# Performance work log

Measured on AMD Instinct MI355X. Metric: run time of the kernel, lower is better.

The kernel has to match this reference:

```python
import jax, jax.numpy as jnp
import numpy as np

D = 64
NEG = 0.01            # leakyrelu_neg_slope
X_CONN = 0.25         # x_connection_init
SKIP_H = 0.5          # skip_weight_h
SIGMAS = np.asarray(1.5 ** np.arange(15), np.float32)  # all_sigmas_dist

N_LIG, N_REC = 4096, 8192
E_LIG, E_REC = 65536, 262144
F_LIG, F_REC, NRBF = 15, 27, 15


def _lrelu(x):
    return jax.nn.leaky_relu(x, NEG)


def _ln(x, g, b, eps=1e-5):
    m = x.mean(-1, keepdims=True)
    v = ((x - m) ** 2).mean(-1, keepdims=True)
    return (x - m) * jax.lax.rsqrt(v + eps) * g + b


def _mlp2(x, w1, b1, g, bt, w2, b2):
    # nn.Sequential(Linear, Dropout(0), LeakyReLU, LayerNorm, Linear) in eval mode
    return _ln(_lrelu(x @ w1 + b1), g, bt) @ w2 + b2


def _coords_mlp(m, w1, b1, w2, b2):
    # nn.Sequential(Linear, Dropout(0), LeakyReLU, Linear(out,1))
    return _lrelu(m @ w1 + b1) @ w2 + b2  # [E, 1]


def _seg_mean(v, idx, n):
    # DGL fn.mean over incoming edges at destination nodes (0 for isolated nodes)
    s = jax.ops.segment_sum(v, idx, num_segments=n)
    c = jax.ops.segment_sum(jnp.ones(idx.shape, v.dtype), idx, num_segments=n)
    return s / jnp.maximum(c, 1.0)[:, None]


def setup_inputs() -> dict:
    key = jax.random.key(0)
    ks = iter(jax.random.split(key, 64))

    def n(shape, s=1.0):
        return jax.random.normal(next(ks), shape, jnp.float32) * s

    def lin(i, o):
        return n((i, o), 1.0 / float(np.sqrt(i)))

    zeros = lambda *s: jnp.zeros(s, jnp.float32)
    ones = lambda *s: jnp.ones(s, jnp.float32)

    d = {}
    d['coords_lig'] = n((N_LIG, 3))
    d['h_lig'] = n((N_LIG, D))
    d['orig_h_lig'] = n((N_LIG, D))
    d['orig_coords_lig'] = n((N_LIG, 3))
    d['coords_rec'] = n((N_REC, 3))
    d['h_rec'] = n((N_REC, D))
    d['orig_h_rec'] = n((N_REC, D))
    d['orig_coords_rec'] = n((N_REC, 3))
    d['lig_src'] = jax.random.randint(next(ks), (E_LIG,), 0, N_LIG)
    d['lig_dst'] = jax.random.randint(next(ks), (E_LIG,), 0, N_LIG)
    d['lig_efeat'] = n((E_LIG, F_LIG))
    d['rec_src'] = jax.random.randint(next(ks), (E_REC,), 0, N_REC)
    d['rec_dst'] = jax.random.randint(next(ks), (E_REC,), 0, N_REC)
    d['rec_efeat'] = n((E_REC, F_REC))
    d['mask'] = (jax.random.uniform(next(ks), (N_LIG, N_REC)) < 0.5).astype(jnp.float32)
    # ---- parameters ----
    d['lig_em_w1'], d['lig_em_b1'] = lin(2 * D + F_LIG + NRBF, D), zeros(D)
    d['lig_em_g'], d['lig_em_bt'] = ones(D), zeros(D)
    d['lig_em_w2'], d['lig_em_b2'] = lin(D, D), zeros(D)
    d['rec_em_w1'], d['rec_em_b1'] = lin(2 * D + F_REC + NRBF, D), zeros(D)
    d['rec_em_g'], d['rec_em_bt'] = ones(D), zeros(D)
    d['rec_em_w2'], d['rec_em_b2'] = lin(D, D), zeros(D)
    d['lig_cm_w1'], d['lig_cm_b1'] = lin(D, D), zeros(D)
    d['lig_cm_w2'], d['lig_cm_b2'] = lin(D, 1), zeros(1)
    d['rec_cm_w1'], d['rec_cm_b1'] = lin(D, D), zeros(D)
    d['rec_cm_w2'], d['rec_cm_b2'] = lin(D, 1), zeros(1)
    for nm in ['q_lig_w', 'k_lig_w', 'v_lig_w', 'q_rec_w', 'k_rec_w', 'v_rec_w']:
        d[nm] = lin(D, D)
    d['lig_nm_w1'], d['lig_nm_b1'] = lin(4 * D, D), zeros(D)
    d['lig_nm_g'], d['lig_nm_bt'] = ones(D), zeros(D)
    d['lig_nm_w2'], d['lig_nm_b2'] = lin(D, D), zeros(D)
    d['rec_nm_w1'], d['rec_nm_b1'] = lin(4 * D, D), zeros(D)
    d['rec_nm_g'], d['rec_nm_bt'] = ones(D), zeros(D)
    d['rec_nm_w2'], d['rec_nm_b2'] = lin(D, D), zeros(D)
    return d


def reference(coords_lig, h_lig, orig_h_lig, orig_coords_lig,
              coords_rec, h_rec, orig_h_rec, orig_coords_rec,
              lig_src, lig_dst, lig_efeat, rec_src, rec_dst, rec_efeat, mask,
              lig_em_w1, lig_em_b1, lig_em_g, lig_em_bt, lig_em_w2, lig_em_b2,
              rec_em_w1, rec_em_b1, rec_em_g, rec_em_bt, rec_em_w2, rec_em_b2,
              lig_cm_w1, lig_cm_b1, lig_cm_w2, lig_cm_b2,
              rec_cm_w1, rec_cm_b1, rec_cm_w2, rec_cm_b2,
              q_lig_w, k_lig_w, v_lig_w, q_rec_w, k_rec_w, v_rec_w,
              lig_nm_w1, lig_nm_b1, lig_nm_g, lig_nm_bt, lig_nm_w2, lig_nm_b2,
              rec_nm_w1, rec_nm_b1, rec_nm_g, rec_nm_bt, rec_nm_w2, rec_nm_b2):
    n_lig, n_rec = coords_lig.shape[0], coords_rec.shape[0]
    sig = jnp.asarray(SIGMAS, coords_lig.dtype)

    # --- ligand edge messages: x_rel = x_src - x_dst, multi-scale RBF of |x_rel|^2 ---
    xr_l = coords_lig[lig_src] - coords_lig[lig_dst]                       # [E_l, 3]
    rbf_l = jnp.exp(-jnp.sum(xr_l * xr_l, -1, keepdims=True) / sig)        # [E_l, 15]
    msg_l = _mlp2(jnp.concatenate([h_lig[lig_src], h_lig[lig_dst], lig_efeat, rbf_l], -1),
                  lig_em_w1, lig_em_b1, lig_em_g, lig_em_bt, lig_em_w2, lig_em_b2)

    # --- receptor edge messages (rec_square_distance_scale = 1) ---
    xr_r = coords_rec[rec_src] - coords_rec[rec_dst]
    rbf_r = jnp.exp(-jnp.sum(xr_r * xr_r, -1, keepdims=True) / sig)
    msg_r = _mlp2(jnp.concatenate([h_rec[rec_src], h_rec[rec_dst], rec_efeat, rbf_r], -1),
                  rec_em_w1, rec_em_b1, rec_em_g, rec_em_bt, rec_em_w2, rec_em_b2)

    # --- masked cross-graph attention (pre/post cross-msg norms are identity) ---
    q_l, k_l, v_l = _lrelu(h_lig @ q_lig_w), _lrelu(h_lig @ k_lig_w), h_lig @ v_lig_w
    q_r, k_r, v_r = _lrelu(h_rec @ q_rec_w), _lrelu(h_rec @ k_rec_w), h_rec @ v_rec_w
    s_lr = mask * (q_l @ k_r.T) - 1000.0 * (1.0 - mask)
    att_l = jax.nn.softmax(s_lr, axis=1) @ v_r                             # [N_l, D]
    mt = mask.T
    s_rl = mt * (q_r @ k_l.T) - 1000.0 * (1.0 - mt)
    att_r = jax.nn.softmax(s_rl, axis=1) @ v_l                             # [N_r, D]

    # --- equivariant coordinate update: mean_j phi_x(m_ij) * x_rel, + skip to orig ---
    coef_l = _coords_mlp(msg_l, lig_cm_w1, lig_cm_b1, lig_cm_w2, lig_cm_b2)
    x_lig = X_CONN * orig_coords_lig + (1.0 - X_CONN) * coords_lig + _seg_mean(xr_l * coef_l, lig_dst, n_lig)
    coef_r = _coords_mlp(msg_r, rec_cm_w1, rec_cm_b1, rec_cm_w2, rec_cm_b2)
    x_rec = X_CONN * orig_coords_rec + (1.0 - X_CONN) * coords_rec + _seg_mean(xr_r * coef_r, rec_dst, n_rec)

    # --- node feature update with skip (h_feats_dim == out_feats_dim) ---
    aggr_l = _seg_mean(msg_l, lig_dst, n_lig)
    h_lig_out = SKIP_H * _mlp2(jnp.concatenate([h_lig, aggr_l, att_l, orig_h_lig], -1),
                               lig_nm_w1, lig_nm_b1, lig_nm_g, lig_nm_bt, lig_nm_w2, lig_nm_b2) \
        + (1.0 - SKIP_H) * h_lig
    aggr_r = _seg_mean(msg_r, rec_dst, n_rec)
    h_rec_out = SKIP_H * _mlp2(jnp.concatenate([h_rec, aggr_r, att_r, orig_h_rec], -1),
                               rec_nm_w1, rec_nm_b1, rec_nm_g, rec_nm_bt, rec_nm_w2, rec_nm_b2) \
        + (1.0 - SKIP_H) * h_rec
    return x_lig, h_lig_out, x_rec, h_rec_out
```

## Files before the change

kernel.cpp:

```cpp
#include <hip/hip_runtime.h>
#include <hip/hip_bf16.h>

typedef __hip_bfloat16 bf16;
typedef __attribute__((ext_vector_type(8))) short bfrag8;
typedef __attribute__((ext_vector_type(4))) float f32x4;

#define N_LIG 4096
#define N_REC 8192
#define E_LIG 65536
#define E_REC 262144
#define F_LIGc 15
#define F_RECc 27

__device__ __forceinline__ float ldkv(const float* p, size_t i) { return p[i]; }
__device__ __forceinline__ float ldkv(const bf16* p, size_t i) { return __bfloat162float(p[i]); }
__device__ __forceinline__ short bfbits(float x) {
    bf16 b = __float2bfloat16(x);
    return *(short*)&b;
}
__device__ __forceinline__ unsigned short stg(const float* p, size_t i) {
    return (unsigned short)bfbits(p[i]);
}
__device__ __forceinline__ unsigned short stg(const bf16* p, size_t i) {
    return *(const unsigned short*)(p + i);
// ... 21 lines not shown
    0.1316872428f, 0.08779149520f, 0.05852766346f, 0.03901844231f,
    0.02601229487f, 0.01734152992f, 0.01156101994f, 0.007707346628f,
    0.005138231085f, 0.003425487390f};

__device__ __forceinline__ float wave_sum(float v) {
    #pragma unroll
    for (int o = 32; o > 0; o >>= 1) v += __shfl_xor(v, o, 64);
    return v;
}
__device__ __forceinline__ float quad_max(float v) {
    v = fmaxf(v, __shfl_xor(v, 1)); v = fmaxf(v, __shfl_xor(v, 2));
    v = fmaxf(v, __shfl_xor(v, 4)); v = fmaxf(v, __shfl_xor(v, 8));
    return v;
}

__global__ void zero_kernel(float* __restrict__ p, int n) {
    int i = blockIdx.x * blockDim.x + threadIdx.x;
    if (i < n) p[i] = 0.f;
}

__global__ void cvt4_kernel(
    const float* __restrict__ a, bf16* __restrict__ oa, int na,
    const float* __restrict__ b, bf16* __restrict__ ob, int nb,
    const float* __restrict__ c, bf16* __restrict__ oc, int nc,
    const float* __restrict__ d, bf16* __restrict__ od, int nd)
{
    int i = blockIdx.x * 256 + threadIdx.x;
    if (i < na) { oa[i] = __float2bfloat16(a[i]); return; }
    i -= na;
    if (i < nb) { ob[i] = __float2bfloat16(b[i]); return; }
    i -= nb;
    if (i < nc) { oc[i] = __float2bfloat16(c[i]); return; }
    i -= nc;
    if (i < nd) od[i] = __float2bfloat16(d[i]);
}

__global__ void hist2_kernel(const int* __restrict__ dl, const int* __restrict__ dr,
                             int* __restrict__ cl, int* __restrict__ cr) {
    int i = blockIdx.x * 256 + threadIdx.x;
    if (i < E_LIG) { atomicAdd(&cl[dl[i]], 1); return; }
    i -= E_LIG;
    if (i < E_REC) atomicAdd(&cr[dr[i]], 1);
}

__global__ __launch_bounds__(256) void scan2_kernel(
    const int* __restrict__ cl, int* __restrict__ curl,
    const int* __restrict__ cr, int* __restrict__ curr)
{
    const int* counts = blockIdx.x ? cr : cl;
    int* cursor = blockIdx.x ? curr : curl;
    int n = blockIdx.x ? N_REC : N_LIG;
    __shared__ int part[256];
    int t = threadIdx.x;
    int c = n / 256;
    int base = t * c;
    int s = 0;
    for (int i = 0; i < c; ++i) s += counts[base + i];
// ... 7 lines not shown
    }
    int run = part[t] - s;
    for (int i = 0; i < c; ++i) {
        cursor[base + i] = run;
        run += counts[base + i];
    }
}

__global__ void scatter2_kernel(const int* __restrict__ dl, const int* __restrict__ dr,
                                int* __restrict__ curl, int* __restrict__ curr,
                                int* __restrict__ ordl, int* __restrict__ ordr) {
    int i = blockIdx.x * 256 + threadIdx.x;
    if (i < E_LIG) { ordl[atomicAdd(&curl[dl[i]], 1)] = i; return; }
    i -= E_LIG;
    if (i < E_REC) ordr[atomicAdd(&curr[dr[i]], 1)] = i;
}

__global__ __launch_bounds__(256) void pack_frags(
    const float* __restrict__ w_rec1, const float* __restrict__ w_lig1,
    const float* __restrict__ w_rec2, const float* __restrict__ w_lig2,
    const float* __restrict__ c_rec1, const float* __restrict__ c_lig1,
    unsigned short* __restrict__ p_rec1, unsigned short* __restrict__ p_lig1,
    unsigned short* __restrict__ p_rec2, unsigned short* __restrict__ p_lig2,
    unsigned short* __restrict__ pc_rec1, unsigned short* __restrict__ pc_lig1)
{
    int b = blockIdx.x;
    const float* src; unsigned short* dst; int kk, IN;
    if (b < 6)       { src = w_rec1; dst = p_rec1;  kk = b;      IN = 170; }
    else if (b < 11) { src = w_lig1; dst = p_lig1;  kk = b - 6;  IN = 158; }
    else if (b < 13) { src = w_rec2; dst = p_rec2;  kk = b - 11; IN = 64; }
    else if (b < 15) { src = w_lig2; dst = p_lig2;  kk = b - 13; IN = 64; }
    else if (b < 17) { src = c_rec1; dst = pc_rec1; kk = b - 15; IN = 64; }
    else             { src = c_lig1; dst = pc_lig1; kk = b - 17; IN = 64; }
    int t = threadIdx.x, wv = t >> 6, L = t & 63, lm = L & 15, qd = L >> 4;
    int n = wv * 16 + lm;
    unsigned short tmp[8];
    #pragma unroll
    for (int j = 0; j < 8; ++j) {
        int k = kk * 32 + qd * 8 + j;
        tmp[j] = (k < IN) ? (unsigned short)bfbits(src[k * 64 + n]) : (unsigned short)0;
    }
    *(uint4*)&dst[((size_t)(kk * 4 + wv) * 64 + L) * 8] = *(uint4*)tmp;
}

template <int F, int K1S, typename HT>
__device__ __forceinline__ void edge_body(
    char* sbuf, int ebid,
    const int* __restrict__ order,
    const float* __restrict__ coords, const HT* __restrict__ h,
    const int* __restrict__ src, const int* __restrict__ dst,
    const HT* __restrict__ efeat,
    const unsigned short* __restrict__ w1p, const float* __restrict__ b1,
    const float* __restrict__ g, const float* __restrict__ bt,
    const unsigned short* __restrict__ w2p, const float* __restrict__ b2,
    const unsigned short* __restrict__ c1p, const float* __restrict__ cb1,
    const float* __restrict__ cw2, const float* __restrict__ cb2,
    float* __restrict__ aggr, float* __restrict__ xacc)
// ... 220 lines not shown
    const float *h, *qw, *mf;
    const bf16 *kkp, *vvp;
    const unsigned long long* mq;
    long mrs, mcs;
    float *pO, *pM, *pL;
    int n_rows, n_cols, nsplit;
    if (bid < nb1) {
        h = h1; qw = qw1; kkp = k1; vvp = v1; mq = mq1; mf = mf1; mrs = mrs1; mcs = mcs1;
        pO = pO1; pM = pM1; pL = pL1; n_rows = nrows1; n_cols = ncols1; nsplit = nsplit1;
    } else {
        h = h2; qw = qw2; kkp = k2; vvp = v2; mq = mq2; mf = mf2; mrs = mrs2; mcs = mcs2;
        pO = pO2; pM = pM2; pL = pL2; n_rows = nrows2; n_cols = ncols2; nsplit = nsplit2;
        bid -= nb1;
    }

    unsigned short* sQ = (unsigned short*)sbuf;
    unsigned short* sP = (unsigned short*)(sbuf + 8192);
    unsigned short* sK = (unsigned short*)(sbuf + 16384);
    unsigned short* sV = (unsigned short*)(sbuf + 24576);
    uint2* mtq = (uint2*)(sbuf + 32768);
    unsigned char* mt = (unsigned char*)(sbuf + 32768);

    const int t  = threadIdx.x;
    const int wv = t >> 6;
    const int lm = t & 15;
    const int qd = (t & 63) >> 4;
    const int rb = bid / nsplit;
    const int sp = bid - rb * nsplit;
    const int r0 = rb * 64;
    const int cols_per = n_cols / nsplit;
    const int c_begin = sp * cols_per;

    const int cP = t >> 3, segP = (t & 7) * 8;

    #pragma unroll
    for (int u = 0; u < 2; ++u) {
// ... 6 lines not shown
        const float* qp = qw + (size_t)rr * 64 + segP;
        #pragma unroll
        for (int j = 0; j < 8; ++j) sK[swz(segP + j, rr)] = bfbits(qp[j]);
    }

    uint4 kreg[2], vreg[2];
    unsigned long long mregq = 0;
    kreg[0] = *(const uint4*)(kkp + (size_t)(c_begin + cP) * 64 + segP);
    kreg[1] = *(const uint4*)(kkp + (size_t)(c_begin + cP + 32) * 64 + segP);
    vreg[0] = *(const uint4*)(vvp + (size_t)(c_begin + cP) * 64 + segP);
    vreg[1] = *(const uint4*)(vvp + (size_t)(c_begin + cP + 32) * 64 + segP);
    if (MMODE == 0 && t < 64)
        mregq = mq[(size_t)(c_begin >> 6) * n_rows + r0 + t];
    __syncthreads();

    {
        bfrag8 a0 = *(const bfrag8*)&sP[swz(wv * 16 + lm, qd * 8)];
        bfrag8 a1 = *(const bfrag8*)&sP[swz(wv * 16 + lm, 32 + qd * 8)];
        #pragma unroll
        for (int ns = 0; ns < 4; ++ns) {
            f32x4 acc = {0.f, 0.f, 0.f, 0.f};
            bfrag8 b0 = *(const bfrag8*)&sK[swz(ns * 16 + lm, qd * 8)];
            bfrag8 b1 = *(const bfrag8*)&sK[swz(ns * 16 + lm, 32 + qd * 8)];
            acc = __builtin_amdgcn_mfma_f32_16x16x32_bf16(a0, b0, acc, 0, 0, 0);
            acc = __builtin_amdgcn_mfma_f32_16x16x32_bf16(a1, b1, acc, 0, 0, 0);
            #pragma unroll
            for (int r = 0; r < 4; ++r) {
                float v = acc[r];
                v = v > 0.f ? v : 0.01f * v;
                sQ[swz(wv * 16 + qd * 4 + r, ns * 16 + lm)] = bfbits(v);
            }
        }
    }
    __syncthreads();

    float rm[4];
    #pragma unroll
    for (int r = 0; r < 4; ++r) rm[r] = -1e30f;
    f32x4 o[4];
    #pragma unroll
    for (int ds = 0; ds < 4; ++ds) o[ds] = (f32x4){0.f, 0.f, 0.f, 0.f};
    f32x4 osum = {0.f, 0.f, 0.f, 0.f};
    const short ONE = (short)0x3F80;
    const bfrag8 bones = {ONE, ONE, ONE, ONE, ONE, ONE, ONE, ONE};

    const int nt = cols_per / 64;
    for (int tile = 0; tile < nt; ++tile) {
        #pragma unroll
        for (int u = 0; u < 2; ++u) {
// ... 22 lines not shown
            }
        }
        __syncthreads();

        if (tile + 1 < nt) {
            int c0n = c_begin + (tile + 1) * 64;
            kreg[0] = *(const uint4*)(kkp + (size_t)(c0n + cP) * 64 + segP);
            kreg[1] = *(const uint4*)(kkp + (size_t)(c0n + cP + 32) * 64 + segP);
            vreg[0] = *(const uint4*)(vvp + (size_t)(c0n + cP) * 64 + segP);
            vreg[1] = *(const uint4*)(vvp + (size_t)(c0n + cP + 32) * 64 + segP);
            if (MMODE == 0 && t < 64)
                mregq = mq[(size_t)(c0n >> 6) * n_rows + r0 + t];
        }

        f32x4 s[4];
        {
            bfrag8 a0 = *(const bfrag8*)&sQ[swz(wv * 16 + lm, qd * 8)];
            bfrag8 a1 = *(const bfrag8*)&sQ[swz(wv * 16 + lm, 32 + qd * 8)];
            #pragma unroll
            for (int ns = 0; ns < 4; ++ns) {
                f32x4 acc = {0.f, 0.f, 0.f, 0.f};
                bfrag8 b0 = *(const bfrag8*)&sK[swz(ns * 16 + lm, qd * 8)];
                bfrag8 b1 = *(const bfrag8*)&sK[swz(ns * 16 + lm, 32 + qd * 8)];
                acc = __builtin_amdgcn_mfma_f32_16x16x32_bf16(a0, b0, acc, 0, 0, 0);
                acc = __builtin_amdgcn_mfma_f32_16x16x32_bf16(a1, b1, acc, 0, 0, 0);
                s[ns] = acc;
            }
        }

        float alpha[4];
        #pragma unroll
        for (int r = 0; r < 4; ++r) {
            int rloc = wv * 16 + qd * 4 + r;
            float v0, v1, v2, v3;
            if (MMODE == 0) {
                uint2 w = mtq[rloc];
                v0 = (w.x >> lm) & 1        ? s[0][r] : -1000.f;
                v1 = (w.x >> (16 + lm)) & 1 ? s[1][r] : -1000.f;
                v2 = (w.y >> lm) & 1        ? s[2][r] : -1000.f;
                v3 = (w.y >> (16 + lm)) & 1 ? s[3][r] : -1000.f;
            } else {
                v0 = mt[rloc * 80 +  0 + lm] ? s[0][r] : -1000.f;
// ... 42 lines not shown
        #pragma unroll
        for (int r = 0; r < 4; ++r) {
            int row = r0 + wv * 16 + qd * 4 + r;
            pO[((size_t)sp * n_rows + row) * 64 + ds * 16 + lm] = o[ds][r];
        }
    if (lm == 0) {
        #pragma unroll
        for (int r = 0; r < 4; ++r) {
            int row = r0 + wv * 16 + qd * 4 + r;
            pM[(size_t)sp * n_rows + row] = rm[r];
            pL[(size_t)sp * n_rows + row] = osum[r];
        }
    }
}

__global__ __launch_bounds__(256, 4) void mega_kernel(
    int nb1,
    const float* h1, const float* qw1, const bf16* k1, const bf16* v1,
    const unsigned long long* mq1, float* pO1, float* pM1, float* pL1,
    int nrows1, int ncols1, int ns1,
    const float* h2, const float* qw2, const bf16* k2, const bf16* v2,
    const unsigned long long* mq2, float* pO2, float* pM2, float* pL2,
    int nrows2, int ncols2, int ns2,
    const int* ordR, const float* coordsR, const bf16* hR,
    const int* srcR, const int* dstR, const bf16* efR,
    const unsigned short* w1pR, const float* b1R, const float* gR, const float* btR,
    const unsigned short* w2pR, const float* b2R,
    const unsigned short* c1pR, const float* cb1R, const float* cw2R, const float* cb2R,
    float* aggrR, float* xaccR,
    const int* ordL, const float* coordsL, const bf16* hL,
    const int* srcL, const int* dstL, const bf16* efL,
    const unsigned short* w1pL, const float* b1L, const float* gL, const float* btL,
    const unsigned short* w2pL, const float* b2L,
    const unsigned short* c1pL, const float* cb1L, const float* cw2L, const float* cb2L,
    float* aggrL, float* xaccL)
{
    __shared__ __align__(16) char sbuf[33280];
    int bid = blockIdx.x;
    int g7 = bid / 7, r7 = bid - g7 * 7;
    if (r7 < 2) {
        attn_body<0>(sbuf, g7 * 2 + r7, nb1,
            h1, qw1, k1, v1, mq1, (const float*)0, 0L, 0L, pO1, pM1, pL1, nrows1, ncols1, ns1,
            h2, qw2, k2, v2, mq2, (const float*)0, 0L, 0L, pO2, pM2, pL2, nrows2, ncols2, ns2);
    } else {
        int eid = g7 * 5 + (r7 - 2);
        if (eid < E_REC / 64)
            edge_body<F_RECc, 6, bf16>(sbuf, eid, ordR, coordsR, hR, srcR, dstR, efR,
                w1pR, b1R, gR, btR, w2pR, b2R, c1pR, cb1R, cw2R, cb2R, aggrR, xaccR);
        else
            edge_body<F_LIGc, 5, bf16>(sbuf, eid - E_REC / 64, ordL, coordsL, hL, srcL, dstL, efL,
                w1pL, b1L, gL, btL, w2pL, b2L, c1pL, cb1L, cw2L, cb2L, aggrL, xaccL);
    }
// ... 10 lines not shown
{
    __shared__ __align__(16) char sbuf[64 * (K1S * 32 + 8) * 2 + 5632];
    edge_body<F, K1S, float>(sbuf, blockIdx.x, order, coords, h, src, dst, efeat,
        w1p, b1, g, bt, w2p, b2, c1p, cb1, cw2, cb2, aggr, xacc);
}

__global__ __launch_bounds__(256, 4) void attn_f32mask(
    int nb1,
    const float* h1, const float* qw1, const bf16* k1, const bf16* v1,
    const float* mf1, long mrs1, long mcs1,
    float* pO1, float* pM1, float* pL1, int nrows1, int ncols1, int ns1,
    const float* h2, const float* qw2, const bf16* k2, const bf16* v2,
    const float* mf2, long mrs2, long mcs2,
    float* pO2, float* pM2, float* pL2, int nrows2, int ncols2, int ns2)
{
    __shared__ __align__(16) char sbuf[37888];
    attn_body<1>(sbuf, blockIdx.x, nb1,
        h1, qw1, k1, v1, (const unsigned long long*)0, mf1, mrs1, mcs1,
        pO1, pM1, pL1, nrows1, ncols1, ns1,
        h2, qw2, k2, v2, (const unsigned long long*)0, mf2, mrs2, mcs2,
        pO2, pM2, pL2, nrows2, ncols2, ns2);
}

__global__ __launch_bounds__(256, 3) void node_mfma(
    int nbl, int nbn,
    const float* h1, const float* __restrict__ aggr1, const int* __restrict__ cnt1,
    const float* att1, const float* __restrict__ origh1,
    const float* __restrict__ w1a, const float* __restrict__ b1a,
    const float* __restrict__ ga, const float* __restrict__ bta,
    const float* __restrict__ w2a, const float* __restrict__ b2a, float* out1,
    const float* h2, const float* __restrict__ aggr2, const int* __restrict__ cnt2,
// ... 132 lines not shown
    #pragma unroll
    for (int m = 0; m < 4; ++m) {
        f32x4 acc = {0.f, 0.f, 0.f, 0.f};
        #pragma unroll
        for (int kk = 0; kk < 2; ++kk) {
            bfrag8 a = *(const bfrag8*)&h1b[(m * 16 + lm) * 72 + kk * 32 + qd * 8];
            acc = __builtin_amdgcn_mfma_f32_16x16x32_bf16(a, w2f[kk], acc, 0, 0, 0);
        }
        #pragma unroll
        for (int r = 0; r < 4; ++r) {
            int row = n0 + m * 16 + qd * 4 + r;
            float o = acc[r] + b2n;
            float hv = h[(size_t)row * 64 + n];
            h_out[(size_t)row * 64 + n] = 0.5f * o + 0.5f * hv;
        }
    }
}

__global__ __launch_bounds__(256) void kv_proj_kernel(
    const float* __restrict__ h_lig, const float* __restrict__ h_rec,
    const float* __restrict__ kwl, const float* __restrict__ vwl,
    const float* __restrict__ kwr, const float* __restrict__ vwr,
    bf16* __restrict__ kbl, bf16* __restrict__ vbl,
    bf16* __restrict__ kbr, bf16* __restrict__ vbr)
{
    int job = blockIdx.x * 4 + (threadIdx.x >> 6);
    int j = threadIdx.x & 63;
    const float *h, *w; bf16* out; int node, do_l;
    if (job < N_LIG)                { h = h_lig; w = kwl; out = kbl; node = job;                   do_l = 1; }
    else if (job < 2 * N_LIG)       { h = h_lig; w = vwl; out = vbl; node = job - N_LIG;           do_l = 0; }
    else if (job < 2 * N_LIG + N_REC) { h = h_rec; w = kwr; out = kbr; node = job - 2 * N_LIG;     do_l = 1; }
    else                            { h = h_rec; w = vwr; out = vbr; node = job - 2 * N_LIG - N_REC; do_l = 0; }
    float xv = h[(size_t)node * 64 + j];
    float acc = 0.f;
    #pragma unroll
    for (int i = 0; i < 64; ++i) acc += __shfl(xv, i, 64) * w[i * 64 + j];
    if (do_l) acc = acc > 0.f ? acc : 0.01f * acc;
    out[(size_t)node * 64 + j] = __float2bfloat16(acc);
}

__global__ __launch_bounds__(256) void build_masks(
    const float* __restrict__ mask, unsigned long long* __restrict__ mq,
    unsigned long long* __restrict__ mqT, int R, int C)
{
    __shared__ __align__(4) unsigned char tr[64 * 68];
    __shared__ __align__(4) unsigned char tc[64 * 68];
    int r0 = blockIdx.y * 64, c0 = blockIdx.x * 64;
    int t = threadIdx.x;
    int cs = (t & 15) * 4;
    #pragma unroll
    for (int rr = 0; rr < 4; ++rr) {
        int r = (t >> 4) + rr * 16;
        const float* mp = &mask[(size_t)(r0 + r) * C + c0 + cs];
        unsigned char b0 = mp[0] != 0.f, b1 = mp[1] != 0.f;
        unsigned char b2 = mp[2] != 0.f, b3 = mp[3] != 0.f;
        tr[r * 68 + cs + 0] = b0; tr[r * 68 + cs + 1] = b1;
        tr[r * 68 + cs + 2] = b2; tr[r * 68 + cs + 3] = b3;
        tc[(cs + 0) * 68 + r] = b0; tc[(cs + 1) * 68 + r] = b1;
        tc[(cs + 2) * 68 + r] = b2; tc[(cs + 3) * 68 + r] = b3;
    }
    __syncthreads();
    if (t < 128) {
        const unsigned* p = (t < 64) ? (const unsigned*)&tr[t * 68]
                                     : (const unsigned*)&tc[(t - 64) * 68];
        unsigned lo = 0, hi = 0;
        #pragma unroll
        for (int i = 0; i < 8; ++i)
            lo |= (((p[i] & 0x01010101u) * 0x01020408u) >> 24 & 0xFu) << (4 * i);
        #pragma unroll
        for (int i = 8; i < 16; ++i)
            hi |= (((p[i] & 0x01010101u) * 0x01020408u) >> 24 & 0xFu) << (4 * (i - 8));
        unsigned long long w = (unsigned long long)lo | ((unsigned long long)hi << 32);
        if (t < 64) mq[(size_t)(c0 >> 6) * R + r0 + t] = w;
        else        mqT[(size_t)(r0 >> 6) * C + c0 + (t - 64)] = w;
    }
}

__global__ __launch_bounds__(64) void attn_merge2(
    const float* __restrict__ pO1, const float* __restrict__ pM1, const float* __restrict__ pL1,
    float* __restrict__ out1, int ns1,
    const float* __restrict__ pO2, const float* __restrict__ pM2, const float* __restrict__ pL2,
    float* __restrict__ out2, int ns2)
{
    int r = blockIdx.x;
    const float *pO, *pM, *pL; float* out; int n_rows, nsplit;
    if (r < N_LIG) { pO = pO1; pM = pM1; pL = pL1; out = out1; n_rows = N_LIG; nsplit = ns1; }
    else { r -= N_LIG; pO = pO2; pM = pM2; pL = pL2; out = out2; n_rows = N_REC; nsplit = ns2; }
    int d = threadIdx.x;
    float mstar = -1e30f;
// ... 105 lines not shown
    const float *k_rec_w = (const float*)d_in[39], *v_rec_w = (const float*)d_in[40];
    const float *lig_nm_w1 = (const float*)d_in[41], *lig_nm_b1 = (const float*)d_in[42];
    const float *lig_nm_g  = (const float*)d_in[43], *lig_nm_bt = (const float*)d_in[44];
    const float *lig_nm_w2 = (const float*)d_in[45], *lig_nm_b2 = (const float*)d_in[46];
    const float *rec_nm_w1 = (const float*)d_in[47], *rec_nm_b1 = (const float*)d_in[48];
    const float *rec_nm_g  = (const float*)d_in[49], *rec_nm_bt = (const float*)d_in[50];
    const float *rec_nm_w2 = (const float*)d_in[51], *rec_nm_b2 = (const float*)d_in[52];

    char* wsb = (char*)d_ws;
    float* aggr_l = (float*)(wsb + 16);
    float* aggr_r = aggr_l + (size_t)N_LIG * 64;
    float* xacc_l = aggr_r + (size_t)N_REC * 64;
    float* xacc_r = xacc_l + (size_t)N_LIG * 3;
    int* counts_l = (int*)(xacc_r + (size_t)N_REC * 3);
    int* counts_r = counts_l + N_LIG;
    const size_t zero_floats =
        (size_t)N_LIG * 64 + (size_t)N_REC * 64 + N_LIG * 3 + N_REC * 3 + N_LIG + N_REC;
    int* cursor_l = counts_r + N_REC;
    int* cursor_r = cursor_l + N_LIG;
    int* order_l  = cursor_r + N_REC;
    int* order_r  = order_l + E_LIG;
    unsigned short* p_rec1  = (unsigned short*)(order_r + E_REC);
    unsigned short* p_lig1  = p_rec1 + 6 * 2048;
    unsigned short* p_rec2  = p_lig1 + 5 * 2048;
    unsigned short* p_lig2  = p_rec2 + 2 * 2048;
    unsigned short* pc_rec1 = p_lig2 + 2 * 2048;
    unsigned short* pc_lig1 = pc_rec1 + 2 * 2048;
    char* kv_base = (char*)(pc_lig1 + 2 * 2048);
    const size_t core_b = (size_t)(kv_base - wsb);
    const size_t kv_b = (size_t)(N_LIG + N_REC) * 64 * 2 * 2;

    const size_t mq1_n = (size_t)(N_REC / 64) * N_LIG;
// ... 28 lines not shown
    float* pM2 = pL1 + (size_t)ns1 * N_LIG;
    float* pL2 = pM2 + (size_t)ns2 * N_REC;
    unsigned long long* mqb  = (unsigned long long*)(kv_base + kv_b + part_b);
    unsigned long long* mqbT = mqb + mq1_n;
    bf16* hb_l  = (bf16*)(mqbT + mq2_n);
    bf16* hb_r  = hb_l + (size_t)N_LIG * 64;
    bf16* efb_l = hb_r + (size_t)N_REC * 64;
    bf16* efb_r = efb_l + (size_t)E_LIG * F_LIGc;

    float* out = (float*)d_out;
    float* x_lig_o = out;
    float* h_lig_o = out + 12288;
    float* x_rec_o = out + 274432;
    float* h_rec_o = out + 299008;

    zero_kernel<<<((int)zero_floats + 255) / 256, 256, 0, stream>>>(aggr_l, (int)zero_floats);

    if (tier == 0) {
        dim3 bg(N_REC / 64, N_LIG / 64);
        build_masks<<<bg, 256, 0, stream>>>(mask, mqb, mqbT, N_LIG, N_REC);
    }

    pack_frags<<<19, 256, 0, stream>>>(
        rec_em_w1, lig_em_w1, rec_em_w2, lig_em_w2, rec_cm_w1, lig_cm_w1,
        p_rec1, p_lig1, p_rec2, p_lig2, pc_rec1, pc_lig1);

    hist2_kernel<<<(E_LIG + E_REC) / 256, 256, 0, stream>>>(lig_dst, rec_dst, counts_l, counts_r);
    scan2_kernel<<<2, 256, 0, stream>>>(counts_l, cursor_l, counts_r, cursor_r);
    scatter2_kernel<<<(E_LIG + E_REC) / 256, 256, 0, stream>>>(
        lig_dst, rec_dst, cursor_l, cursor_r, order_l, order_r);

    kv_proj_kernel<<<(2 * (N_LIG + N_REC)) / 4, 256, 0, stream>>>(
        h_lig, h_rec, k_lig_w, v_lig_w, k_rec_w, v_rec_w,
        kb_l, vb_l, kb_r, vb_r);

    const int nb1 = (N_LIG / 64) * ns1;
    const int nb2 = (N_REC / 64) * ns2;

    if (tier == 0) {
        cvt4_kernel<<<(N_LIG * 64 + N_REC * 64 + E_LIG * F_LIGc + E_REC * F_RECc + 255) / 256,
                      256, 0, stream>>>(
            h_lig, hb_l, N_LIG * 64, h_rec, hb_r, N_REC * 64,
            lig_efeat, efb_l, E_LIG * F_LIGc, rec_efeat, efb_r, E_REC * F_RECc);

        mega_kernel<<<7 * 1024, 256, 0, stream>>>(
            nb1,
            h_lig, q_lig_w, kb_r, vb_r, mqb, pO1, pM1, pL1, N_LIG, N_REC, ns1,
            h_rec, q_rec_w, kb_l, vb_l, mqbT, pO2, pM2, pL2, N_REC, N_LIG, ns2,
            order_r, coords_rec, hb_r, rec_src, rec_dst, efb_r,
            p_rec1, rec_em_b1, rec_em_g, rec_em_bt, p_rec2, rec_em_b2,
            pc_rec1, rec_cm_b1, rec_cm_w2, rec_cm_b2, aggr_r, xacc_r,
            order_l, coords_lig, hb_l, lig_src, lig_dst, efb_l,
            p_lig1, lig_em_b1, lig_em_g, lig_em_bt, p_lig2, lig_em_b2,
            pc_lig1, lig_cm_b1, lig_cm_w2, lig_cm_b2, aggr_l, xacc_l);

        attn_merge2<<<N_LIG + N_REC, 64, 0, stream>>>(
            pO1, pM1, pL1, h_lig_o, ns1, pO2, pM2, pL2, h_rec_o, ns2);
    } else {
        edge_mfma_f<F_LIGc, 5><<<E_LIG / 64, 256, 0, stream>>>(
            order_l, coords_lig, h_lig, lig_src, lig_dst, lig_efeat,
            p_lig1, lig_em_b1, lig_em_g, lig_em_bt, p_lig2, lig_em_b2,
            pc_lig1, lig_cm_b1, lig_cm_w2, lig_cm_b2, aggr_l, xacc_l);
        edge_mfma_f<F_RECc, 6><<<E_REC / 64, 256, 0, stream>>>(
            order_r, coords_rec, h_rec, rec_src, rec_dst, rec_efeat,
            p_rec1, rec_em_b1, rec_em_g, rec_em_bt, p_rec2, rec_em_b2,
            pc_rec1, rec_cm_b1, rec_cm_w2, rec_cm_b2, aggr_r, xacc_r);
        if (tier == 1) {
            attn_f32mask<<<nb1 + nb2, 256, 0, stream>>>(
                nb1,
                h_lig, q_lig_w, kb_r, vb_r, mask, (long)N_REC, 1L,
                pO1, pM1, pL1, N_LIG, N_REC, ns1,
                h_rec, q_rec_w, kb_l, vb_l, mask, 1L, (long)N_REC,
                pO2, pM2, pL2, N_REC, N_LIG, ns2);
// ... 22 lines not shown
```

Baseline: 605.7 us.

## Fuse preprocessing kernels into one launch and shrink attention shared memory

Merges mask bit-packing, bf16 conversion, K/V projection, destination histogram and weight fragment packing into a single prep_kernel on the default tier, cutting several launches and their serialization gaps. The attention body now keeps the Q tile as register fragments loaded once, reusing the sP buffer instead of a separate sQ region. That shrinks shared memory so mega_kernel can raise launch bounds to 5 blocks per CU. The cost is higher register pressure from keeping the Q fragments resident, which may cause spills under the tighter occupancy bound.

```diff
diff --git a/kernel.cpp b/kernel.cpp
--- a/kernel.cpp
+++ b/kernel.cpp
@@ -59,33 +59,180 @@
     return v;
 }
 
+__device__ __forceinline__ void pack_body(
+    int b, int t,
+    const float* w_rec1, const float* w_lig1, const float* w_rec2, const float* w_lig2,
+    const float* c_rec1, const float* c_lig1,
+    unsigned short* p_rec1, unsigned short* p_lig1,
+    unsigned short* p_rec2, unsigned short* p_lig2,
+    unsigned short* pc_rec1, unsigned short* pc_lig1)
+{
+    const float* src; unsigned short* dst; int kk, IN;
+    if (b < 6)       { src = w_rec1; dst = p_rec1;  kk = b;      IN = 170; }
+    else if (b < 11) { src = w_lig1; dst = p_lig1;  kk = b - 6;  IN = 158; }
+    else if (b < 13) { src = w_rec2; dst = p_rec2;  kk = b - 11; IN = 64; }
+    else if (b < 15) { src = w_lig2; dst = p_lig2;  kk = b - 13; IN = 64; }
+    else if (b < 17) { src = c_rec1; dst = pc_rec1; kk = b - 15; IN = 64; }
+    else             { src = c_lig1; dst = pc_lig1; kk = b - 17; IN = 64; }
+    int wv = t >> 6, L = t & 63, lm = L & 15, qd = L >> 4;
+    int n = wv * 16 + lm;
+    unsigned short tmp[8];
+    #pragma unroll
+    for (int j = 0; j < 8; ++j) {
+        int k = kk * 32 + qd * 8 + j;
+        tmp[j] = (k < IN) ? (unsigned short)bfbits(src[k * 64 + n]) : (unsigned short)0;
+    }
+    *(uint4*)&dst[((size_t)(kk * 4 + wv) * 64 + L) * 8] = *(uint4*)tmp;
+}
+
+__device__ __forceinline__ void kv_body(
+    int job, int j,
+    const float* h_lig, const float* h_rec,
+    const float* kwl, const float* vwl, const float* kwr, const float* vwr,
+    bf16* kbl, bf16* vbl, bf16* kbr, bf16* vbr)
+{
+    const float *h, *w; bf16* out; int node, do_l;
+    if (job < N_LIG)                  { h = h_lig; w = kwl; out = kbl; node = job;                     do_l = 1; }
+    else if (job < 2 * N_LIG)         { h = h_lig; w = vwl; out = vbl; node = job - N_LIG;             do_l = 0; }
+    else if (job < 2 * N_LIG + N_REC) { h = h_rec; w = kwr; out = kbr; node = job - 2 * N_LIG;         do_l = 1; }
+    else                              { h = h_rec; w = vwr; out = vbr; node = job - 2 * N_LIG - N_REC; do_l = 0; }
+    float xv = h[(size_t)node * 64 + j];
+    float acc = 0.f;
+    #pragma unroll
+    for (int i = 0; i < 64; ++i) acc += __shfl(xv, i, 64) * w[i * 64 + j];
+    if (do_l) acc = acc > 0.f ? acc : 0.01f * acc;
+    out[(size_t)node * 64 + j] = __float2bfloat16(acc);
+}
+
+__device__ __forceinline__ void mask_body(
+    unsigned char* tr, unsigned char* tc, int bx, int by, int t,
+    const float* mask, unsigned long long* mq, unsigned long long* mqT, int R, int C)
+{
+    int r0 = by * 64, c0 = bx * 64;
+    int cs = (t & 15) * 4;
+    #pragma unroll
+    for (int rr = 0; rr < 4; ++rr) {
+        int r = (t >> 4) + rr * 16;
+        const float* mp = &mask[(size_t)(r0 + r) * C + c0 + cs];
+        unsigned char b0 = mp[0] != 0.f, b1 = mp[1] != 0.f;
+        unsigned char b2 = mp[2] != 0.f, b3 = mp[3] != 0.f;
+        tr[r * 68 + cs + 0] = b0; tr[r * 68 + cs + 1] = b1;
+        tr[r * 68 + cs + 2] = b2; tr[r * 68 + cs + 3] = b3;
+        tc[(cs + 0) * 68 + r] = b0; tc[(cs + 1) * 68 + r] = b1;
+        tc[(cs + 2) * 68 + r] = b2; tc[(cs + 3) * 68 + r] = b3;
+    }
+    __syncthreads();
+    if (t < 128) {
+        const unsigned* p = (t < 64) ? (const unsigned*)&tr[t * 68]
+                                     : (const unsigned*)&tc[(t - 64) * 68];
+        unsigned lo = 0, hi = 0;
+        #pragma unroll
+        for (int i = 0; i < 8; ++i)
+            lo |= (((p[i] & 0x01010101u) * 0x01020408u) >> 24 & 0xFu) << (4 * i);
+        #pragma unroll
+        for (int i = 8; i < 16; ++i)
+            hi |= (((p[i] & 0x01010101u) * 0x01020408u) >> 24 & 0xFu) << (4 * (i - 8));
+        unsigned long long w = (unsigned long long)lo | ((unsigned long long)hi << 32);
+        if (t < 64) mq[(size_t)(c0 >> 6) * R + r0 + t] = w;
+        else        mqT[(size_t)(r0 >> 6) * C + c0 + (t - 64)] = w;
+    }
+}
+
+#define NB_MASK  ((N_REC / 64) * (N_LIG / 64))
+#define N_CVT    (N_LIG * 64 + N_REC * 64 + E_LIG * F_LIGc + E_REC * F_RECc)
+#define NB_CVT   (N_CVT / 256)
+#define NB_KV    (2 * (N_LIG + N_REC) / 4)
+#define N_ZERO   (N_LIG * 64 + N_REC * 64 + N_LIG * 3 + N_REC * 3 + N_LIG + N_REC)
+#define NB_HIST  ((E_LIG + E_REC) / 256)
+#define NB_PACK  19
+#define NB_PREP  (NB_MASK + NB_CVT + NB_KV + NB_HIST + NB_PACK)
+
+__global__ __launch_bounds__(256) void prep_kernel(
+    const float* __restrict__ mask, unsigned long long* __restrict__ mq,
+    unsigned long long* __restrict__ mqT,
+    const float* __restrict__ h_lig, bf16* __restrict__ hb_l,
+    const float* __restrict__ h_rec, bf16* __restrict__ hb_r,
+    const float* __restrict__ ef_l, bf16* __restrict__ efb_l,
+    const float* __restrict__ ef_r, bf16* __restrict__ efb_r,
+    const float* __restrict__ kwl, const float* __restrict__ vwl,
+    const float* __restrict__ kwr, const float* __restrict__ vwr,
+    bf16* __restrict__ kbl, bf16* __restrict__ vbl,
+    bf16* __restrict__ kbr, bf16* __restrict__ vbr,
+    const int* __restrict__ dl, const int* __restrict__ dr,
+    int* __restrict__ cl, int* __restrict__ cr,
+    const float* w_rec1, const float* w_lig1, const float* w_rec2, const float* w_lig2,
+    const float* c_rec1, const float* c_lig1,
+    unsigned short* p_rec1, unsigned short* p_lig1,
+    unsigned short* p_rec2, unsigned short* p_lig2,
+    unsigned short* pc_rec1, unsigned short* pc_lig1)
+{
+    __shared__ unsigned char tr[64 * 68];
+    __shared__ unsigned char tc[64 * 68];
+    int b = blockIdx.x, t = threadIdx.x;
+    if (b < NB_MASK) {
+        mask_body(tr, tc, b & 127, b >> 7, t, mask, mq, mqT, N_LIG, N_REC);
+        return;
+    }
+    b -= NB_MASK;
+    if (b < NB_CVT) {
+        int i = b * 256 + t;
+        if (i < N_LIG * 64) { hb_l[i] = __float2bfloat16(h_lig[i]); return; }
+        i -= N_LIG * 64;
+        if (i < N_REC * 64) { hb_r[i] = __float2bfloat16(h_rec[i]); return; }
+        i -= N_REC * 64;
+        if (i < E_LIG * F_LIGc) { efb_l[i] = __float2bfloat16(ef_l[i]); return; }
+        i -= E_LIG * F_LIGc;
+        efb_r[i] = __float2bfloat16(ef_r[i]);
+        return;
+    }
+    b -= NB_CVT;
+    if (b < NB_KV) {
+        kv_body(b * 4 + (t >> 6), t & 63, h_lig, h_rec, kwl, vwl, kwr, vwr,
+                kbl, vbl, kbr, vbr);
+        return;
+    }
+    b -= NB_KV;
+    if (b < NB_HIST) {
+        int i = b * 256 + t;
+        if (i < E_LIG) atomicAdd(&cl[dl[i]], 1);
+        else atomicAdd(&cr[dr[i - E_LIG]], 1);
+        return;
+    }
+    b -= NB_HIST;
+    pack_body(b, t, w_rec1, w_lig1, w_rec2, w_lig2, c_rec1, c_lig1,
+              p_rec1, p_lig1, p_rec2, p_lig2, pc_rec1, pc_lig1);
+}
+
 __global__ void zero_kernel(float* __restrict__ p, int n) {
     int i = blockIdx.x * blockDim.x + threadIdx.x;
     if (i < n) p[i] = 0.f;
 }
-
-__global__ void cvt4_kernel(
-    const float* __restrict__ a, bf16* __restrict__ oa, int na,
-    const float* __restrict__ b, bf16* __restrict__ ob, int nb,
-    const float* __restrict__ c, bf16* __restrict__ oc, int nc,
-    const float* __restrict__ d, bf16* __restrict__ od, int nd)
-{
-    int i = blockIdx.x * 256 + threadIdx.x;
-    if (i < na) { oa[i] = __float2bfloat16(a[i]); return; }
-    i -= na;
-    if (i < nb) { ob[i] = __float2bfloat16(b[i]); return; }
-    i -= nb;
-    if (i < nc) { oc[i] = __float2bfloat16(c[i]); return; }
-    i -= nc;
-    if (i < nd) od[i] = __float2bfloat16(d[i]);
-}
-
 __global__ void hist2_kernel(const int* __restrict__ dl, const int* __restrict__ dr,
                              int* __restrict__ cl, int* __restrict__ cr) {
     int i = blockIdx.x * 256 + threadIdx.x;
     if (i < E_LIG) { atomicAdd(&cl[dl[i]], 1); return; }
     i -= E_LIG;
     if (i < E_REC) atomicAdd(&cr[dr[i]], 1);
+}
+__global__ __launch_bounds__(256) void pack_frags(
+    const float* w_rec1, const float* w_lig1, const float* w_rec2, const float* w_lig2,
+    const float* c_rec1, const float* c_lig1,
+    unsigned short* p_rec1, unsigned short* p_lig1,
+    unsigned short* p_rec2, unsigned short* p_lig2,
+    unsigned short* pc_rec1, unsigned short* pc_lig1)
+{
+    pack_body(blockIdx.x, threadIdx.x, w_rec1, w_lig1, w_rec2, w_lig2, c_rec1, c_lig1,
+              p_rec1, p_lig1, p_rec2, p_lig2, pc_rec1, pc_lig1);
+}
+__global__ __launch_bounds__(256) void kv_proj_kernel(
+    const float* __restrict__ h_lig, const float* __restrict__ h_rec,
+    const float* __restrict__ kwl, const float* __restrict__ vwl,
+    const float* __restrict__ kwr, const float* __restrict__ vwr,
+    bf16* __restrict__ kbl, bf16* __restrict__ vbl,
+    bf16* __restrict__ kbr, bf16* __restrict__ vbr)
+{
+    kv_body(blockIdx.x * 4 + (threadIdx.x >> 6), threadIdx.x & 63,
+            h_lig, h_rec, kwl, vwl, kwr, vwr, kbl, vbl, kbr, vbr);
 }
 
 __global__ __launch_bounds__(256) void scan2_kernel(
@@ -123,33 +270,6 @@
     if (i < E_LIG) { ordl[atomicAdd(&curl[dl[i]], 1)] = i; return; }
     i -= E_LIG;
     if (i < E_REC) ordr[atomicAdd(&curr[dr[i]], 1)] = i;
-}
-
-__global__ __launch_bounds__(256) void pack_frags(
-    const float* __restrict__ w_rec1, const float* __restrict__ w_lig1,
-    const float* __restrict__ w_rec2, const float* __restrict__ w_lig2,
-    const float* __restrict__ c_rec1, const float* __restrict__ c_lig1,
-    unsigned short* __restrict__ p_rec1, unsigned short* __restrict__ p_lig1,
-    unsigned short* __restrict__ p_rec2, unsigned short* __restrict__ p_lig2,
-    unsigned short* __restrict__ pc_rec1, unsigned short* __restrict__ pc_lig1)
-{
-    int b = blockIdx.x;
-    const float* src; unsigned short* dst; int kk, IN;
-    if (b < 6)       { src = w_rec1; dst = p_rec1;  kk = b;      IN = 170; }
-    else if (b < 11) { src = w_lig1; dst = p_lig1;  kk = b - 6;  IN = 158; }
-    else if (b < 13) { src = w_rec2; dst = p_rec2;  kk = b - 11; IN = 64; }
-    else if (b < 15) { src = w_lig2; dst = p_lig2;  kk = b - 13; IN = 64; }
-    else if (b < 17) { src = c_rec1; dst = pc_rec1; kk = b - 15; IN = 64; }
-    else             { src = c_lig1; dst = pc_lig1; kk = b - 17; IN = 64; }
-    int t = threadIdx.x, wv = t >> 6, L = t & 63, lm = L & 15, qd = L >> 4;
-    int n = wv * 16 + lm;
-    unsigned short tmp[8];
-    #pragma unroll
-    for (int j = 0; j < 8; ++j) {
-        int k = kk * 32 + qd * 8 + j;
-        tmp[j] = (k < IN) ? (unsigned short)bfbits(src[k * 64 + n]) : (unsigned short)0;
-    }
-    *(uint4*)&dst[((size_t)(kk * 4 + wv) * 64 + L) * 8] = *(uint4*)tmp;
 }
 
 template <int F, int K1S, typename HT>
@@ -400,12 +520,11 @@
         bid -= nb1;
     }
 
-    unsigned short* sQ = (unsigned short*)sbuf;
-    unsigned short* sP = (unsigned short*)(sbuf + 8192);
-    unsigned short* sK = (unsigned short*)(sbuf + 16384);
-    unsigned short* sV = (unsigned short*)(sbuf + 24576);
-    uint2* mtq = (uint2*)(sbuf + 32768);
-    unsigned char* mt = (unsigned char*)(sbuf + 32768);
+    unsigned short* sP = (unsigned short*)sbuf;
+    unsigned short* sK = (unsigned short*)(sbuf + 8192);
+    unsigned short* sV = (unsigned short*)(sbuf + 16384);
+    uint2* mtq = (uint2*)(sbuf + 24576);
+    unsigned char* mt = (unsigned char*)(sbuf + 24576);
 
     const int t  = threadIdx.x;
     const int wv = t >> 6;
@@ -442,6 +561,7 @@
         mregq = mq[(size_t)(c_begin >> 6) * n_rows + r0 + t];
     __syncthreads();
 
+    float qv[4][4];
     {
         bfrag8 a0 = *(const bfrag8*)&sP[swz(wv * 16 + lm, qd * 8)];
         bfrag8 a1 = *(const bfrag8*)&sP[swz(wv * 16 + lm, 32 + qd * 8)];
@@ -455,12 +575,20 @@
             #pragma unroll
             for (int r = 0; r < 4; ++r) {
                 float v = acc[r];
-                v = v > 0.f ? v : 0.01f * v;
-                sQ[swz(wv * 16 + qd * 4 + r, ns * 16 + lm)] = bfbits(v);
+                qv[ns][r] = v > 0.f ? v : 0.01f * v;
             }
         }
     }
     __syncthreads();
+
+    #pragma unroll
+    for (int ns = 0; ns < 4; ++ns)
+        #pragma unroll
+        for (int r = 0; r < 4; ++r)
+            sP[swz(wv * 16 + qd * 4 + r, ns * 16 + lm)] = bfbits(qv[ns][r]);
+    __syncthreads();
+    bfrag8 aq0 = *(const bfrag8*)&sP[swz(wv * 16 + lm, qd * 8)];
+    bfrag8 aq1 = *(const bfrag8*)&sP[swz(wv * 16 + lm, 32 + qd * 8)];
 
     float rm[4];
     #pragma unroll
@@ -513,18 +641,14 @@
         }
 
         f32x4 s[4];
-        {
-            bfrag8 a0 = *(const bfrag8*)&sQ[swz(wv * 16 + lm, qd * 8)];
-            bfrag8 a1 = *(const bfrag8*)&sQ[swz(wv * 16 + lm, 32 + qd * 8)];
-            #pragma unroll
-            for (int ns = 0; ns < 4; ++ns) {
-                f32x4 acc = {0.f, 0.f, 0.f, 0.f};
-                bfrag8 b0 = *(const bfrag8*)&sK[swz(ns * 16 + lm, qd * 8)];
-                bfrag8 b1 = *(const bfrag8*)&sK[swz(ns * 16 + lm, 32 + qd * 8)];
-                acc = __builtin_amdgcn_mfma_f32_16x16x32_bf16(a0, b0, acc, 0, 0, 0);
-                acc = __builtin_amdgcn_mfma_f32_16x16x32_bf16(a1, b1, acc, 0, 0, 0);
-                s[ns] = acc;
-            }
+        #pragma unroll
+        for (int ns = 0; ns < 4; ++ns) {
+            f32x4 acc = {0.f, 0.f, 0.f, 0.f};
+            bfrag8 b0 = *(const bfrag8*)&sK[swz(ns * 16 + lm, qd * 8)];
+            bfrag8 b1 = *(const bfrag8*)&sK[swz(ns * 16 + lm, 32 + qd * 8)];
+            acc = __builtin_amdgcn_mfma_f32_16x16x32_bf16(aq0, b0, acc, 0, 0, 0);
+            acc = __builtin_amdgcn_mfma_f32_16x16x32_bf16(aq1, b1, acc, 0, 0, 0);
+            s[ns] = acc;
         }
 
         float alpha[4];
@@ -597,7 +721,7 @@
     }
 }
 
-__global__ __launch_bounds__(256, 4) void mega_kernel(
+__global__ __launch_bounds__(256, 5) void mega_kernel(
     int nb1,
     const float* h1, const float* qw1, const bf16* k1, const bf16* v1,
     const unsigned long long* mq1, float* pO1, float* pM1, float* pL1,
@@ -618,7 +742,7 @@
     const unsigned short* c1pL, const float* cb1L, const float* cw2L, const float* cb2L,
     float* aggrL, float* xaccL)
 {
-    __shared__ __align__(16) char sbuf[33280];
+    __shared__ __align__(16) char sbuf[31232];
     int bid = blockIdx.x;
     int g7 = bid / 7, r7 = bid - g7 * 7;
     if (r7 < 2) {
@@ -659,7 +783,7 @@
     const float* mf2, long mrs2, long mcs2,
     float* pO2, float* pM2, float* pL2, int nrows2, int ncols2, int ns2)
 {
-    __shared__ __align__(16) char sbuf[37888];
+    __shared__ __align__(16) char sbuf[29696];
     attn_body<1>(sbuf, blockIdx.x, nb1,
         h1, qw1, k1, v1, (const unsigned long long*)0, mf1, mrs1, mcs1,
         pO1, pM1, pL1, nrows1, ncols1, ns1,
@@ -822,65 +946,6 @@
             float hv = h[(size_t)row * 64 + n];
             h_out[(size_t)row * 64 + n] = 0.5f * o + 0.5f * hv;
         }
-    }
-}
-
-__global__ __launch_bounds__(256) void kv_proj_kernel(
-    const float* __restrict__ h_lig, const float* __restrict__ h_rec,
-    const float* __restrict__ kwl, const float* __restrict__ vwl,
-    const float* __restrict__ kwr, const float* __restrict__ vwr,
-    bf16* __restrict__ kbl, bf16* __restrict__ vbl,
-    bf16* __restrict__ kbr, bf16* __restrict__ vbr)
-{
-    int job = blockIdx.x * 4 + (threadIdx.x >> 6);
-    int j = threadIdx.x & 63;
-    const float *h, *w; bf16* out; int node, do_l;
-    if (job < N_LIG)                { h = h_lig; w = kwl; out = kbl; node = job;                   do_l = 1; }
-    else if (job < 2 * N_LIG)       { h = h_lig; w = vwl; out = vbl; node = job - N_LIG;           do_l = 0; }
-    else if (job < 2 * N_LIG + N_REC) { h = h_rec; w = kwr; out = kbr; node = job - 2 * N_LIG;     do_l = 1; }
-    else                            { h = h_rec; w = vwr; out = vbr; node = job - 2 * N_LIG - N_REC; do_l = 0; }
-    float xv = h[(size_t)node * 64 + j];
-    float acc = 0.f;
-    #pragma unroll
-    for (int i = 0; i < 64; ++i) acc += __shfl(xv, i, 64) * w[i * 64 + j];
-    if (do_l) acc = acc > 0.f ? acc : 0.01f * acc;
-    out[(size_t)node * 64 + j] = __float2bfloat16(acc);
-}
-
-__global__ __launch_bounds__(256) void build_masks(
-    const float* __restrict__ mask, unsigned long long* __restrict__ mq,
-    unsigned long long* __restrict__ mqT, int R, int C)
-{
-    __shared__ __align__(4) unsigned char tr[64 * 68];
-    __shared__ __align__(4) unsigned char tc[64 * 68];
-    int r0 = blockIdx.y * 64, c0 = blockIdx.x * 64;
-    int t = threadIdx.x;
-    int cs = (t & 15) * 4;
-    #pragma unroll
-    for (int rr = 0; rr < 4; ++rr) {
-        int r = (t >> 4) + rr * 16;
-        const float* mp = &mask[(size_t)(r0 + r) * C + c0 + cs];
-        unsigned char b0 = mp[0] != 0.f, b1 = mp[1] != 0.f;
-        unsigned char b2 = mp[2] != 0.f, b3 = mp[3] != 0.f;
-        tr[r * 68 + cs + 0] = b0; tr[r * 68 + cs + 1] = b1;
-        tr[r * 68 + cs + 2] = b2; tr[r * 68 + cs + 3] = b3;
-        tc[(cs + 0) * 68 + r] = b0; tc[(cs + 1) * 68 + r] = b1;
-        tc[(cs + 2) * 68 + r] = b2; tc[(cs + 3) * 68 + r] = b3;
-    }
-    __syncthreads();
-    if (t < 128) {
-        const unsigned* p = (t < 64) ? (const unsigned*)&tr[t * 68]
-                                     : (const unsigned*)&tc[(t - 64) * 68];
-        unsigned lo = 0, hi = 0;
-        #pragma unroll
-        for (int i = 0; i < 8; ++i)
-            lo |= (((p[i] & 0x01010101u) * 0x01020408u) >> 24 & 0xFu) << (4 * i);
-        #pragma unroll
-        for (int i = 8; i < 16; ++i)
-            hi |= (((p[i] & 0x01010101u) * 0x01020408u) >> 24 & 0xFu) << (4 * (i - 8));
-        unsigned long long w = (unsigned long long)lo | ((unsigned long long)hi << 32);
-        if (t < 64) mq[(size_t)(c0 >> 6) * R + r0 + t] = w;
-        else        mqT[(size_t)(r0 >> 6) * C + c0 + (t - 64)] = w;
     }
 }
 
@@ -1016,8 +1081,6 @@
     float* xacc_r = xacc_l + (size_t)N_LIG * 3;
     int* counts_l = (int*)(xacc_r + (size_t)N_REC * 3);
     int* counts_r = counts_l + N_LIG;
-    const size_t zero_floats =
-        (size_t)N_LIG * 64 + (size_t)N_REC * 64 + N_LIG * 3 + N_REC * 3 + N_LIG + N_REC;
     int* cursor_l = counts_r + N_REC;
     int* cursor_r = cursor_l + N_LIG;
     int* order_l  = cursor_r + N_REC;
@@ -1076,34 +1139,21 @@
     float* x_rec_o = out + 274432;
     float* h_rec_o = out + 299008;
 
-    zero_kernel<<<((int)zero_floats + 255) / 256, 256, 0, stream>>>(aggr_l, (int)zero_floats);
-
-    if (tier == 0) {
-        dim3 bg(N_REC / 64, N_LIG / 64);
-        build_masks<<<bg, 256, 0, stream>>>(mask, mqb, mqbT, N_LIG, N_REC);
-    }
-
-    pack_frags<<<19, 256, 0, stream>>>(
-        rec_em_w1, lig_em_w1, rec_em_w2, lig_em_w2, rec_cm_w1, lig_cm_w1,
-        p_rec1, p_lig1, p_rec2, p_lig2, pc_rec1, pc_lig1);
-
-    hist2_kernel<<<(E_LIG + E_REC) / 256, 256, 0, stream>>>(lig_dst, rec_dst, counts_l, counts_r);
-    scan2_kernel<<<2, 256, 0, stream>>>(counts_l, cursor_l, counts_r, cursor_r);
-    scatter2_kernel<<<(E_LIG + E_REC) / 256, 256, 0, stream>>>(
-        lig_dst, rec_dst, cursor_l, cursor_r, order_l, order_r);
-
-    kv_proj_kernel<<<(2 * (N_LIG + N_REC)) / 4, 256, 0, stream>>>(
-        h_lig, h_rec, k_lig_w, v_lig_w, k_rec_w, v_rec_w,
-        kb_l, vb_l, kb_r, vb_r);
-
     const int nb1 = (N_LIG / 64) * ns1;
     const int nb2 = (N_REC / 64) * ns2;
 
     if (tier == 0) {
-        cvt4_kernel<<<(N_LIG * 64 + N_REC * 64 + E_LIG * F_LIGc + E_REC * F_RECc + 255) / 256,
-                      256, 0, stream>>>(
-            h_lig, hb_l, N_LIG * 64, h_rec, hb_r, N_REC * 64,
-            lig_efeat, efb_l, E_LIG * F_LIGc, rec_efeat, efb_r, E_REC * F_RECc);
+        zero_kernel<<<(N_ZERO + 255) / 256, 256, 0, stream>>>(aggr_l, N_ZERO);
+        prep_kernel<<<NB_PREP, 256, 0, stream>>>(
+            mask, mqb, mqbT,
+            h_lig, hb_l, h_rec, hb_r, lig_efeat, efb_l, rec_efeat, efb_r,
+            k_lig_w, v_lig_w, k_rec_w, v_rec_w, kb_l, vb_l, kb_r, vb_r,
+            lig_dst, rec_dst, counts_l, counts_r,
+            rec_em_w1, lig_em_w1, rec_em_w2, lig_em_w2, rec_cm_w1, lig_cm_w1,
+            p_rec1, p_lig1, p_rec2, p_lig2, pc_rec1, pc_lig1);
+        scan2_kernel<<<2, 256, 0, stream>>>(counts_l, cursor_l, counts_r, cursor_r);
+        scatter2_kernel<<<(E_LIG + E_REC) / 256, 256, 0, stream>>>(
+            lig_dst, rec_dst, cursor_l, cursor_r, order_l, order_r);
 
         mega_kernel<<<7 * 1024, 256, 0, stream>>>(
             nb1,
@@ -1119,6 +1169,19 @@
         attn_merge2<<<N_LIG + N_REC, 64, 0, stream>>>(
             pO1, pM1, pL1, h_lig_o, ns1, pO2, pM2, pL2, h_rec_o, ns2);
     } else {
+        zero_kernel<<<(N_ZERO + 255) / 256, 256, 0, stream>>>(aggr_l, N_ZERO);
+        pack_frags<<<19, 256, 0, stream>>>(
+            rec_em_w1, lig_em_w1, rec_em_w2, lig_em_w2, rec_cm_w1, lig_cm_w1,
+            p_rec1, p_lig1, p_rec2, p_lig2, pc_rec1, pc_lig1);
+        hist2_kernel<<<(E_LIG + E_REC) / 256, 256, 0, stream>>>(
+            lig_dst, rec_dst, counts_l, counts_r);
+        scan2_kernel<<<2, 256, 0, stream>>>(counts_l, cursor_l, counts_r, cursor_r);
+        scatter2_kernel<<<(E_LIG + E_REC) / 256, 256, 0, stream>>>(
+            lig_dst, rec_dst, cursor_l, cursor_r, order_l, order_r);
+        kv_proj_kernel<<<(2 * (N_LIG + N_REC)) / 4, 256, 0, stream>>>(
+            h_lig, h_rec, k_lig_w, v_lig_w, k_rec_w, v_rec_w,
+            kb_l, vb_l, kb_r, vb_r);
+
         edge_mfma_f<F_LIGc, 5><<<E_LIG / 64, 256, 0, stream>>>(
             order_l, coords_lig, h_lig, lig_src, lig_dst, lig_efeat,
             p_lig1, lig_em_b1, lig_em_g, lig_em_bt, p_lig2, lig_em_b2,
```

After: 646.4 us. 6.7% more time.
